# Performance work log

Hardware: AMD Instinct MI355X
Metric: run time of the kernel (lower is better)

## Reference

```python
import jax, jax.numpy as jnp
import numpy as np

ALPHA = 0.2  # LeakyReLU negative slope
NEG_INF = -9e15


def setup_inputs() -> dict:
    key = jax.random.key(0)
    k1, k2, k3, k4 = jax.random.split(key, 4)
    N, IN_F, OUT_F, H = 8192, 256, 128, 2
    HD = OUT_F // H
    h = jax.random.normal(k1, (N, IN_F), dtype=jnp.float32)
    adj = jax.random.randint(k2, (N, N), 0, 2, dtype=jnp.int32)
    # xavier_uniform with gain=1.414
    g = 1.414
    limW = g * np.sqrt(6.0 / (IN_F + HD))
    W = jax.random.uniform(k3, (H, IN_F, HD), jnp.float32, -limW, limW)
    lima = g * np.sqrt(6.0 / (2 * HD + 1))
    a = jax.random.uniform(k4, (H, 2 * HD, 1), jnp.float32, -lima, lima)
    return {"h": h, "adj": adj, "W": W, "a": a}


def reference(h, adj, W, a):
    # Wh: (H, N, HD)
    Wh = jnp.einsum('ni,hid->hnd', h, W)
    HD = W.shape[-1]
    a1 = a[:, :HD, 0]   # (H, HD) -> applied to Wh_i
    a2 = a[:, HD:, 0]   # (H, HD) -> applied to Wh_j
    # a . [Wh_i || Wh_j] == a1.Wh_i + a2.Wh_j ; avoids the (N,N,2HD) tensor
    f1 = jnp.einsum('hnd,hd->hn', Wh, a1)  # (H, N)
    f2 = jnp.einsum('hnd,hd->hn', Wh, a2)  # (H, N)
    e = jax.nn.leaky_relu(f1[:, :, None] + f2[:, None, :], ALPHA)  # (H, N, N)
    mask = (adj > 0)[None, :, :]
    e = jnp.where(mask, e, NEG_INF)
    attention = jax.nn.softmax(e, axis=-1)  # (H, N, N)
    # dropout is identity in eval mode
    h_prime = jnp.einsum('hnm,hmd->hnd', attention, Wh)  # (H, N, HD)
    N = h.shape[0]
    h_prime = jnp.transpose(h_prime, (1, 0, 2)).reshape(N, -1)  # concat heads
    return jax.nn.elu(h_prime)
```

## Files before the change

### kernel.cpp

```cpp
#include <hip/hip_runtime.h>
#include <stdint.h>

#define N_NODES 8192
#define IN_F    256
#define HD      64
#define NH      2
#define MS      4
#define NT      ((N_NODES / MS) / 64)
#define ALPHA   0.2f

typedef __attribute__((ext_vector_type(8))) short bf16x8s;
typedef __attribute__((ext_vector_type(4))) float f32x4;

#define OFF_U      0
#define OFF_WFRAG  4096
#define OFF_F1     69632
#define OFF_F2     135168
#define OFF_F2MAX  200704
#define OFF_G2     200960
#define OFF_WHB    332032
#define OFF_OP     2429184
#define OFF_LP     19206400

__device__ __forceinline__ unsigned short f2bf(float x) {
  union { float f; uint32_t u; } c; c.f = x;
  uint32_t r = c.u + 0x7FFFu + ((c.u >> 16) & 1u);
  return (unsigned short)(r >> 16);
}

__global__ void gat_prep_kernel(const float* __restrict__ W, const float* __restrict__ a,
                                float* __restrict__ u, unsigned short* __restrict__ wfrag)
{
  int idx = blockIdx.x * 256 + threadIdx.x;
  if (idx < 32768) {
    int j = idx & 7, lane = (idx >> 3) & 63, ks = (idx >> 9) & 7, Dt = idx >> 12;
    int k  = ks * 32 + ((lane >> 4) << 3) + j;
    int dp = Dt * 16 + (lane & 15);
    int hh = dp >> 6, d = dp & 63;
    wfrag[idx] = f2bf(W[(size_t)(hh * IN_F + k) * HD + d]);
  } else if (idx < 32768 + NH * 2 * IN_F) {
    int i2 = idx - 32768;
    int i = i2 & 255, v = (i2 >> 8) & 1, h = i2 >> 9;
    const float* Wp = W + (size_t)(h * IN_F + i) * HD;
    const float* ap = a + h * 2 * HD + v * HD;
    float s = 0.f;
    for (int d = 0; d < HD; ++d) s += Wp[d] * ap[d];
    u[(h * 2 + v) * IN_F + i] = s;
  }
}

__global__ __launch_bounds__(256) void gat_f12_kernel(const float* __restrict__ hmat,
    const float* __restrict__ u, float* __restrict__ f1, float* __restrict__ f2,
    float2* __restrict__ g2)
{
  int n = blockIdx.x * 4 + (threadIdx.x >> 6);
  int l = threadIdx.x & 63;
  float4 hv = *(const float4*)(hmat + (size_t)n * IN_F + l * 4);
  float s[4];
#pragma unroll
  for (int q = 0; q < 4; ++q) {
    float4 uv = *(const float4*)(u + q * IN_F + l * 4);
    s[q] = hv.x * uv.x + hv.y * uv.y + hv.z * uv.z + hv.w * uv.w;
  }
#pragma unroll
  for (int off = 1; off < 64; off <<= 1) {
#pragma unroll
    for (int q = 0; q < 4; ++q) s[q] += __shfl_xor(s[q], off);
  }
  if (l == 0) {
    f1[n] = s[0];           f2[n] = s[1];
    f1[N_NODES + n] = s[2]; f2[N_NODES + n] = s[3];
    g2[n]           = make_float2(__expf(s[1]), __expf(ALPHA * s[1]));
    g2[N_NODES + n] = make_float2(__expf(s[3]), __expf(ALPHA * s[3]));
  }
}

__global__ void gat_f2max_kernel(const float* __restrict__ f2, float* __restrict__ f2m)
{
  int h = blockIdx.x;
  float m = -1e30f;
  for (int i = threadIdx.x; i < N_NODES; i += 256) m = fmaxf(m, f2[h * N_NODES + i]);
#pragma unroll
  for (int off = 1; off < 64; off <<= 1) m = fmaxf(m, __shfl_xor(m, off));
  __shared__ float red[4];
  if ((threadIdx.x & 63) == 0) red[threadIdx.x >> 6] = m;
  __syncthreads();
  if (threadIdx.x == 0) f2m[h] = fmaxf(fmaxf(red[0], red[1]), fmaxf(red[2], red[3]));
}

__global__ __launch_bounds__(256) void gat_wh_kernel(const float* __restrict__ hmat,
    const unsigned short* __restrict__ wfrag, unsigned short* __restrict__ whb)
{
  int tid = threadIdx.x;
  int w = tid >> 6, l = tid & 63;
  int n0 = blockIdx.x * 64;
  int row = n0 + w * 16 + (l & 15);
  f32x4 acc[8] = {};
#pragma unroll
  for (int ks = 0; ks < 8; ++ks) {
    const float* ap = hmat + (size_t)row * IN_F + ks * 32 + ((l >> 4) << 3);
    float av[8];
    *(float4*)&av[0] = *(const float4*)ap;
    *(float4*)&av[4] = *(const float4*)(ap + 4);
    bf16x8s af;
#pragma unroll
    for (int j = 0; j < 8; ++j) af[j] = (short)f2bf(av[j]);
#pragma unroll
    for (int Dt = 0; Dt < 8; ++Dt) {
      bf16x8s bfv = *(const bf16x8s*)(wfrag + ((size_t)(Dt * 8 + ks) * 64 + l) * 8);
      acc[Dt] = __builtin_amdgcn_mfma_f32_16x16x32_bf16(af, bfv, acc[Dt], 0, 0, 0);
    }
  }
  int Tm = blockIdx.x;
  int s  = w >> 1;
  int lb = ((w & 1) * 2 + ((l >> 4) >> 1)) * 16 + (l & 15);
  int jh = (l >> 4) & 1;
#pragma unroll
  for (int Dt = 0; Dt < 8; ++Dt) {
    int hh = Dt >> 2, D = Dt & 3;
    ushort4 pk;
    pk.x = f2bf(acc[Dt][0]); pk.y = f2bf(acc[Dt][1]);
    pk.z = f2bf(acc[Dt][2]); pk.w = f2bf(acc[Dt][3]);
    size_t off = ((((size_t)(hh * 128 + Tm) * 2 + s) * 4 + D) * 64 + lb) * 8 + jh * 4;
    *(ushort4*)(whb + off) = pk;
  }
}

__global__ __launch_bounds__(256) void gat_attn_kernel(
    const int* __restrict__ adj, const unsigned short* __restrict__ whb,
    const float* __restrict__ f1, const float2* __restrict__ g2,
    const float* __restrict__ f2max, float* __restrict__ Opart, float* __restrict__ Lpart)
{
  int bx = blockIdx.x;
  int split = bx & (MS - 1);
  int T = bx >> 2;
  int tid = threadIdx.x;
  int w = tid >> 6, l = tid & 63;
  int n0 = T * 64;
  int row = n0 + w * 16 + (l & 15);
  int mbase = split * (N_NODES / MS);
  int koff = (l >> 4) << 3;

  float E1[NH], Ea[NH];
#pragma unroll
  for (int h = 0; h < NH; ++h) {
    float f1v = f1[h * N_NODES + row];
    float tm  = f1v + f2max[h];
    float mrow = fmaxf(tm, ALPHA * tm);
    E1[h] = __expf(f1v - mrow);
    Ea[h] = __expf(ALPHA * f1v - mrow);
  }

  __shared__ float4 gl[2048];
  __shared__ uint4  wbuf[1024];

  {
    const float4* s0 = (const float4*)(g2 + mbase);
    const float4* s1 = (const float4*)(g2 + N_NODES + mbase);
#pragma unroll
    for (int i = 0; i < 4; ++i) {
      gl[i * 256 + tid]        = s0[i * 256 + tid];
      gl[1024 + i * 256 + tid] = s1[i * 256 + tid];
    }
  }

  const int* adjr = adj + (size_t)row * N_NODES + mbase + koff;
  const uint4* ws0 = (const uint4*)(whb + ((size_t)(0 * 128 + (mbase >> 6))) * 4096);
  const uint4* ws1 = (const uint4*)(whb + ((size_t)(1 * 128 + (mbase >> 6))) * 4096);

  int4 raA0 = *(const int4*)(adjr);      int4 raA1 = *(const int4*)(adjr + 4);
  int4 raA2 = *(const int4*)(adjr + 32); int4 raA3 = *(const int4*)(adjr + 36);
  int4 raB0 = *(const int4*)(adjr + 64); int4 raB1 = *(const int4*)(adjr + 68);
  int4 raB2 = *(const int4*)(adjr + 96); int4 raB3 = *(const int4*)(adjr + 100);
  uint4 rw0 = ws0[tid], rw1 = ws0[tid + 256];
  uint4 rw2 = ws1[tid], rw3 = ws1[tid + 256];

  f32x4 acc[NH][4] = {};
  float lsum[NH] = {0.f, 0.f};

#pragma unroll 2
  for (int mt = 0; mt < NT; ++mt) {
    __syncthreads();
    wbuf[tid]       = rw0; wbuf[tid + 256] = rw1;
    wbuf[tid + 512] = rw2; wbuf[tid + 768] = rw3;

    int aj[16];
    *(int4*)&aj[0]  = raA0; *(int4*)&aj[4]  = raA1;
    *(int4*)&aj[8]  = raA2; *(int4*)&aj[12] = raA3;
    raA0 = raB0; raA1 = raB1; raA2 = raB2; raA3 = raB3;
    if (mt + 2 < NT) {
      const int* ap = adjr + (mt + 2) * 64;
      raB0 = *(const int4*)ap;        raB1 = *(const int4*)(ap + 4);
      raB2 = *(const int4*)(ap + 32); raB3 = *(const int4*)(ap + 36);
    }
    if (mt + 1 < NT) {
      const uint4* wp0 = ws0 + (size_t)(mt + 1) * 512;
      const uint4* wp1 = ws1 + (size_t)(mt + 1) * 512;
      rw0 = wp0[tid]; rw1 = wp0[tid + 256];
      rw2 = wp1[tid]; rw3 = wp1[tid + 256];
    }
    __syncthreads();

#pragma unroll
    for (int h = 0; h < NH; ++h) {
      float E1h = E1[h], Eah = Ea[h];
      bf16x8s af[2];
#pragma unroll
      for (int s = 0; s < 2; ++s) {
        const float4* gp = &gl[h * 1024 + ((mt * 64 + s * 32 + koff) >> 1)];
        float ps = 0.f;
#pragma unroll
        for (int k = 0; k < 4; ++k) {
          float4 gv = gp[k];
          int a0 = aj[s * 8 + 2 * k], a1 = aj[s * 8 + 2 * k + 1];
          float p0 = (a0 > 0) ? fmaxf(E1h * gv.x, Eah * gv.y) : 0.f;
          float p1 = (a1 > 0) ? fmaxf(E1h * gv.z, Eah * gv.w) : 0.f;
          ps += p0 + p1;
          af[s][2 * k]     = (short)f2bf(p0);
          af[s][2 * k + 1] = (short)f2bf(p1);
        }
        lsum[h] += ps;
      }
      const unsigned short* lb = (const unsigned short*)wbuf + h * 4096;
#pragma unroll
      for (int s = 0; s < 2; ++s)
#pragma unroll
        for (int D = 0; D < 4; ++D) {
          bf16x8s bfv = *(const bf16x8s*)&lb[(s * 4 + D) * 512 + l * 8];
          acc[h][D] = __builtin_amdgcn_mfma_f32_16x16x32_bf16(af[s], bfv, acc[h][D], 0, 0, 0);
        }
    }
  }

#pragma unroll
  for (int h = 0; h < NH; ++h) {
    float ls = lsum[h];
    ls += __shfl_xor(ls, 16);
    ls += __shfl_xor(ls, 32);
    if (l < 16) Lpart[((size_t)(split * NH + h) << 13) + n0 + w * 16 + l] = ls;
    float* op = Opart + (size_t)(split * NH + h) * N_NODES * HD;
#pragma unroll
    for (int D = 0; D < 4; ++D)
#pragma unroll
      for (int r = 0; r < 4; ++r) {
        int orow = n0 + w * 16 + ((l >> 4) << 2) + r;
        op[(size_t)orow * HD + D * 16 + (l & 15)] = acc[h][D][r];
      }
  }
}

__global__ __launch_bounds__(256) void gat_final_kernel(const float* __restrict__ Opart,
    const float* __restrict__ Lpart, float* __restrict__ out)
{
  int idx = blockIdx.x * 256 + threadIdx.x;
  int n = idx >> 7, c = idx & 127;
  int h = c >> 6, d = c & 63;
  float v = 0.f, ls = 0.f;
#pragma unroll
  for (int sp = 0; sp < MS; ++sp) {
    v  += Opart[((size_t)(sp * NH + h) * N_NODES + n) * HD + d];
    ls += Lpart[(size_t)(sp * NH + h) * N_NODES + n];
  }
  float r = v / fmaxf(ls, 1e-30f);
  out[idx] = (r > 0.f) ? r : (__expf(r) - 1.f);
}

extern "C" void kernel_launch(void* const* d_in, const int* in_sizes, int n_in,
                              void* d_out, int out_size, void* d_ws, size_t ws_size,
                              hipStream_t stream)
{
  const float* hmat = (const float*)d_in[0];
  const int*   adj  = (const int*)d_in[1];
  const float* W    = (const float*)d_in[2];
  const float* a    = (const float*)d_in[3];
  float* out = (float*)d_out;
  char* ws = (char*)d_ws;

  float* u             = (float*)(ws + OFF_U);
  unsigned short* wfrg = (unsigned short*)(ws + OFF_WFRAG);
  float* f1            = (float*)(ws + OFF_F1);
  float* f2            = (float*)(ws + OFF_F2);
  float* f2m           = (float*)(ws + OFF_F2MAX);
  float2* g2           = (float2*)(ws + OFF_G2);
  unsigned short* whb  = (unsigned short*)(ws + OFF_WHB);
  float* Opart         = (float*)(ws + OFF_OP);
  float* Lpart         = (float*)(ws + OFF_LP);

  gat_prep_kernel <<<132, 256, 0, stream>>>(W, a, u, wfrg);
  gat_f12_kernel  <<<N_NODES / 4, 256, 0, stream>>>(hmat, u, f1, f2, g2);
  gat_f2max_kernel<<<NH, 256, 0, stream>>>(f2, f2m);
  gat_wh_kernel   <<<N_NODES / 64, 256, 0, stream>>>(hmat, wfrg, whb);
  gat_attn_kernel <<<128 * MS, 256, 0, stream>>>(adj, whb, f1, g2, f2m, Opart, Lpart);
  gat_final_kernel<<<out_size / 256, 256, 0, stream>>>(Opart, Lpart, out);
}
```

Baseline: 109.8 us.

## Process two row groups per attention block to reuse Wh tiles, double split count

```diff
diff --git a/kernel.cpp b/kernel.cpp
--- a/kernel.cpp
+++ b/kernel.cpp
@@ -1,11 +1,12 @@
 #include <hip/hip_runtime.h>
+#include <hip/hip_bf16.h>
 #include <stdint.h>
 
 #define N_NODES 8192
 #define IN_F    256
 #define HD      64
 #define NH      2
-#define MS      4
+#define MS      8
 #define NT      ((N_NODES / MS) / 64)
 #define ALPHA   0.2f
 
@@ -20,12 +21,16 @@
 #define OFF_G2     200960
 #define OFF_WHB    332032
 #define OFF_OP     2429184
-#define OFF_LP     19206400
+#define OFF_LP     35983616
 
 __device__ __forceinline__ unsigned short f2bf(float x) {
   union { float f; uint32_t u; } c; c.f = x;
   uint32_t r = c.u + 0x7FFFu + ((c.u >> 16) & 1u);
   return (unsigned short)(r >> 16);
+}
+__device__ __forceinline__ short f2bfs(float x) {
+  __hip_bfloat16 b = __float2bfloat16(x);
+  return __builtin_bit_cast(short, b);
 }
 
 __global__ void gat_prep_kernel(const float* __restrict__ W, const float* __restrict__ a,
@@ -104,7 +109,7 @@
     *(float4*)&av[4] = *(const float4*)(ap + 4);
     bf16x8s af;
 #pragma unroll
-    for (int j = 0; j < 8; ++j) af[j] = (short)f2bf(av[j]);
+    for (int j = 0; j < 8; ++j) af[j] = f2bfs(av[j]);
 #pragma unroll
     for (int Dt = 0; Dt < 8; ++Dt) {
       bf16x8s bfv = *(const bf16x8s*)(wfrag + ((size_t)(Dt * 8 + ks) * 64 + l) * 8);
@@ -126,73 +131,68 @@
   }
 }
 
-__global__ __launch_bounds__(256) void gat_attn_kernel(
+#define LOADADJ(d0, d1, d2, d3, p, base) \
+  d0 = *(const int4*)((p) + (base));      d1 = *(const int4*)((p) + (base) + 4); \
+  d2 = *(const int4*)((p) + (base) + 32); d3 = *(const int4*)((p) + (base) + 36);
+
+__global__ __launch_bounds__(256, 2) void gat_attn_kernel(
     const int* __restrict__ adj, const unsigned short* __restrict__ whb,
     const float* __restrict__ f1, const float2* __restrict__ g2,
     const float* __restrict__ f2max, float* __restrict__ Opart, float* __restrict__ Lpart)
 {
   int bx = blockIdx.x;
   int split = bx & (MS - 1);
-  int T = bx >> 2;
+  int T = bx >> 3;
   int tid = threadIdx.x;
   int w = tid >> 6, l = tid & 63;
-  int n0 = T * 64;
-  int row = n0 + w * 16 + (l & 15);
+  int n0 = T * 128;
+  int rbase = n0 + w * 16 + (l & 15);
   int mbase = split * (N_NODES / MS);
   int koff = (l >> 4) << 3;
 
-  float E1[NH], Ea[NH];
-#pragma unroll
-  for (int h = 0; h < NH; ++h) {
-    float f1v = f1[h * N_NODES + row];
-    float tm  = f1v + f2max[h];
-    float mrow = fmaxf(tm, ALPHA * tm);
-    E1[h] = __expf(f1v - mrow);
-    Ea[h] = __expf(ALPHA * f1v - mrow);
-  }
-
-  __shared__ float4 gl[2048];
+  float E1[NH][2], Ea[NH][2];
+#pragma unroll
+  for (int h = 0; h < NH; ++h)
+#pragma unroll
+    for (int rg = 0; rg < 2; ++rg) {
+      float f1v = f1[h * N_NODES + rbase + rg * 64];
+      float tm  = f1v + f2max[h];
+      float mrow = fmaxf(tm, ALPHA * tm);
+      E1[h][rg] = __expf(f1v - mrow);
+      Ea[h][rg] = __expf(ALPHA * f1v - mrow);
+    }
+
+  __shared__ float4 gl[2][512];
   __shared__ uint4  wbuf[1024];
 
   {
     const float4* s0 = (const float4*)(g2 + mbase);
     const float4* s1 = (const float4*)(g2 + N_NODES + mbase);
-#pragma unroll
-    for (int i = 0; i < 4; ++i) {
-      gl[i * 256 + tid]        = s0[i * 256 + tid];
-      gl[1024 + i * 256 + tid] = s1[i * 256 + tid];
-    }
-  }
-
-  const int* adjr = adj + (size_t)row * N_NODES + mbase + koff;
-  const uint4* ws0 = (const uint4*)(whb + ((size_t)(0 * 128 + (mbase >> 6))) * 4096);
-  const uint4* ws1 = (const uint4*)(whb + ((size_t)(1 * 128 + (mbase >> 6))) * 4096);
-
-  int4 raA0 = *(const int4*)(adjr);      int4 raA1 = *(const int4*)(adjr + 4);
-  int4 raA2 = *(const int4*)(adjr + 32); int4 raA3 = *(const int4*)(adjr + 36);
-  int4 raB0 = *(const int4*)(adjr + 64); int4 raB1 = *(const int4*)(adjr + 68);
-  int4 raB2 = *(const int4*)(adjr + 96); int4 raB3 = *(const int4*)(adjr + 100);
+    gl[0][tid] = s0[tid]; gl[0][tid + 256] = s0[tid + 256];
+    gl[1][tid] = s1[tid]; gl[1][tid + 256] = s1[tid + 256];
+  }
+
+  const int* adjr0 = adj + (size_t)rbase * N_NODES + mbase + koff;
+  const int* adjr1 = adjr0 + (size_t)64 * N_NODES;
+  const uint4* ws0 = (const uint4*)(whb + ((size_t)(mbase >> 6)) * 4096);
+  const uint4* ws1 = (const uint4*)(whb + ((size_t)(128 + (mbase >> 6))) * 4096);
+
+  int4 cA0, cA1, cA2, cA3, cB0, cB1, cB2, cB3;
+  int4 nA0, nA1, nA2, nA3, nB0, nB1, nB2, nB3;
+  LOADADJ(cA0, cA1, cA2, cA3, adjr0, 0);
+  LOADADJ(cB0, cB1, cB2, cB3, adjr1, 0);
+  LOADADJ(nA0, nA1, nA2, nA3, adjr0, 64);
+  LOADADJ(nB0, nB1, nB2, nB3, adjr1, 64);
   uint4 rw0 = ws0[tid], rw1 = ws0[tid + 256];
   uint4 rw2 = ws1[tid], rw3 = ws1[tid + 256];
 
-  f32x4 acc[NH][4] = {};
-  float lsum[NH] = {0.f, 0.f};
-
-#pragma unroll 2
+  f32x4 acc[NH][2][4] = {};
+  float lsum[NH][2] = {};
+
   for (int mt = 0; mt < NT; ++mt) {
     __syncthreads();
     wbuf[tid]       = rw0; wbuf[tid + 256] = rw1;
     wbuf[tid + 512] = rw2; wbuf[tid + 768] = rw3;
-
-    int aj[16];
-    *(int4*)&aj[0]  = raA0; *(int4*)&aj[4]  = raA1;
-    *(int4*)&aj[8]  = raA2; *(int4*)&aj[12] = raA3;
-    raA0 = raB0; raA1 = raB1; raA2 = raB2; raA3 = raB3;
-    if (mt + 2 < NT) {
-      const int* ap = adjr + (mt + 2) * 64;
-      raB0 = *(const int4*)ap;        raB1 = *(const int4*)(ap + 4);
-      raB2 = *(const int4*)(ap + 32); raB3 = *(const int4*)(ap + 36);
-    }
     if (mt + 1 < NT) {
       const uint4* wp0 = ws0 + (size_t)(mt + 1) * 512;
       const uint4* wp1 = ws1 + (size_t)(mt + 1) * 512;
@@ -201,25 +201,35 @@
     }
     __syncthreads();
 
+    int ajA[16], ajB[16];
+    *(int4*)&ajA[0] = cA0; *(int4*)&ajA[4]  = cA1;
+    *(int4*)&ajA[8] = cA2; *(int4*)&ajA[12] = cA3;
+    *(int4*)&ajB[0] = cB0; *(int4*)&ajB[4]  = cB1;
+    *(int4*)&ajB[8] = cB2; *(int4*)&ajB[12] = cB3;
+
 #pragma unroll
     for (int h = 0; h < NH; ++h) {
-      float E1h = E1[h], Eah = Ea[h];
-      bf16x8s af[2];
+      bf16x8s afA[2], afB[2];
 #pragma unroll
       for (int s = 0; s < 2; ++s) {
-        const float4* gp = &gl[h * 1024 + ((mt * 64 + s * 32 + koff) >> 1)];
-        float ps = 0.f;
+        const float4* gp = &gl[h][(mt * 64 + s * 32 + koff) >> 1];
+        float psA = 0.f, psB = 0.f;
 #pragma unroll
         for (int k = 0; k < 4; ++k) {
           float4 gv = gp[k];
-          int a0 = aj[s * 8 + 2 * k], a1 = aj[s * 8 + 2 * k + 1];
-          float p0 = (a0 > 0) ? fmaxf(E1h * gv.x, Eah * gv.y) : 0.f;
-          float p1 = (a1 > 0) ? fmaxf(E1h * gv.z, Eah * gv.w) : 0.f;
-          ps += p0 + p1;
-          af[s][2 * k]     = (short)f2bf(p0);
-          af[s][2 * k + 1] = (short)f2bf(p1);
+          float m1x = E1[h][0] * gv.x, max_ = Ea[h][0] * gv.y;
+          float pA0 = (ajA[s * 8 + 2 * k]     > 0) ? fmaxf(m1x, max_) : 0.f;
+          float m1z = E1[h][0] * gv.z, maz = Ea[h][0] * gv.w;
+          float pA1 = (ajA[s * 8 + 2 * k + 1] > 0) ? fmaxf(m1z, maz) : 0.f;
+          float n1x = E1[h][1] * gv.x, nax = Ea[h][1] * gv.y;
+          float pB0 = (ajB[s * 8 + 2 * k]     > 0) ? fmaxf(n1x, nax) : 0.f;
+          float n1z = E1[h][1] * gv.z, naz = Ea[h][1] * gv.w;
+          float pB1 = (ajB[s * 8 + 2 * k + 1] > 0) ? fmaxf(n1z, naz) : 0.f;
+          psA += pA0 + pA1;  psB += pB0 + pB1;
+          afA[s][2 * k] = f2bfs(pA0); afA[s][2 * k + 1] = f2bfs(pA1);
+          afB[s][2 * k] = f2bfs(pB0); afB[s][2 * k + 1] = f2bfs(pB1);
         }
-        lsum[h] += ps;
+        lsum[h][0] += psA; lsum[h][1] += psB;
       }
       const unsigned short* lb = (const unsigned short*)wbuf + h * 4096;
 #pragma unroll
@@ -227,26 +237,36 @@
 #pragma unroll
         for (int D = 0; D < 4; ++D) {
           bf16x8s bfv = *(const bf16x8s*)&lb[(s * 4 + D) * 512 + l * 8];
-          acc[h][D] = __builtin_amdgcn_mfma_f32_16x16x32_bf16(af[s], bfv, acc[h][D], 0, 0, 0);
+          acc[h][0][D] = __builtin_amdgcn_mfma_f32_16x16x32_bf16(afA[s], bfv, acc[h][0][D], 0, 0, 0);
+          acc[h][1][D] = __builtin_amdgcn_mfma_f32_16x16x32_bf16(afB[s], bfv, acc[h][1][D], 0, 0, 0);
         }
     }
-  }
-
-#pragma unroll
-  for (int h = 0; h < NH; ++h) {
-    float ls = lsum[h];
-    ls += __shfl_xor(ls, 16);
-    ls += __shfl_xor(ls, 32);
-    if (l < 16) Lpart[((size_t)(split * NH + h) << 13) + n0 + w * 16 + l] = ls;
-    float* op = Opart + (size_t)(split * NH + h) * N_NODES * HD;
-#pragma unroll
-    for (int D = 0; D < 4; ++D)
-#pragma unroll
-      for (int r = 0; r < 4; ++r) {
-        int orow = n0 + w * 16 + ((l >> 4) << 2) + r;
-        op[(size_t)orow * HD + D * 16 + (l & 15)] = acc[h][D][r];
-      }
-  }
+
+    cA0 = nA0; cA1 = nA1; cA2 = nA2; cA3 = nA3;
+    cB0 = nB0; cB1 = nB1; cB2 = nB2; cB3 = nB3;
+    if (mt + 2 < NT) {
+      LOADADJ(nA0, nA1, nA2, nA3, adjr0, (mt + 2) * 64);
+      LOADADJ(nB0, nB1, nB2, nB3, adjr1, (mt + 2) * 64);
+    }
+  }
+
+#pragma unroll
+  for (int h = 0; h < NH; ++h)
+#pragma unroll
+    for (int rg = 0; rg < 2; ++rg) {
+      float ls = lsum[h][rg];
+      ls += __shfl_xor(ls, 16);
+      ls += __shfl_xor(ls, 32);
+      if (l < 16) Lpart[((size_t)(split * NH + h) << 13) + n0 + rg * 64 + w * 16 + l] = ls;
+      float* op = Opart + (size_t)(split * NH + h) * N_NODES * HD;
+#pragma unroll
+      for (int D = 0; D < 4; ++D)
+#pragma unroll
+        for (int r = 0; r < 4; ++r) {
+          int orow = n0 + rg * 64 + w * 16 + ((l >> 4) << 2) + r;
+          op[(size_t)orow * HD + D * 16 + (l & 15)] = acc[h][rg][D][r];
+        }
+    }
 }
 
 __global__ __launch_bounds__(256) void gat_final_kernel(const float* __restrict__ Opart,
@@ -290,6 +310,6 @@
   gat_f12_kernel  <<<N_NODES / 4, 256, 0, stream>>>(hmat, u, f1, f2, g2);
   gat_f2max_kernel<<<NH, 256, 0, stream>>>(f2, f2m);
   gat_wh_kernel   <<<N_NODES / 64, 256, 0, stream>>>(hmat, wfrg, whb);
-  gat_attn_kernel <<<128 * MS, 256, 0, stream>>>(adj, whb, f1, g2, f2m, Opart, Lpart);
+  gat_attn_kernel <<<64 * MS, 256, 0, stream>>>(adj, whb, f1, g2, f2m, Opart, Lpart);
   gat_final_kernel<<<out_size / 256, 256, 0, stream>>>(Opart, Lpart, out);
 }
```

After: 109.4 us. No clear change (-0.3%).

## Double the column splits and read Wh fragments straight from global memory

Applied to the files above, without the earlier changes.

```diff
diff --git a/kernel.cpp b/kernel.cpp
--- a/kernel.cpp
+++ b/kernel.cpp
@@ -1,12 +1,14 @@
 #include <hip/hip_runtime.h>
+#include <hip/hip_bf16.h>
 #include <stdint.h>
 
 #define N_NODES 8192
 #define IN_F    256
 #define HD      64
 #define NH      2
-#define MS      4
-#define NT      ((N_NODES / MS) / 64)
+#define MS      8
+#define SLICE   1024
+#define NT      16
 #define ALPHA   0.2f
 
 typedef __attribute__((ext_vector_type(8))) short bf16x8s;
@@ -20,12 +22,16 @@
 #define OFF_G2     200960
 #define OFF_WHB    332032
 #define OFF_OP     2429184
-#define OFF_LP     19206400
+#define OFF_LP     35983616
 
 __device__ __forceinline__ unsigned short f2bf(float x) {
   union { float f; uint32_t u; } c; c.f = x;
   uint32_t r = c.u + 0x7FFFu + ((c.u >> 16) & 1u);
   return (unsigned short)(r >> 16);
+}
+__device__ __forceinline__ short f2bfs(float x) {
+  __hip_bfloat16 b = __float2bfloat16(x);
+  return __builtin_bit_cast(short, b);
 }
 
 __global__ void gat_prep_kernel(const float* __restrict__ W, const float* __restrict__ a,
@@ -104,7 +110,7 @@
     *(float4*)&av[4] = *(const float4*)(ap + 4);
     bf16x8s af;
 #pragma unroll
-    for (int j = 0; j < 8; ++j) af[j] = (short)f2bf(av[j]);
+    for (int j = 0; j < 8; ++j) af[j] = f2bfs(av[j]);
 #pragma unroll
     for (int Dt = 0; Dt < 8; ++Dt) {
       bf16x8s bfv = *(const bf16x8s*)(wfrag + ((size_t)(Dt * 8 + ks) * 64 + l) * 8);
@@ -126,20 +132,30 @@
   }
 }
 
-__global__ __launch_bounds__(256) void gat_attn_kernel(
+__global__ __launch_bounds__(256, 3) void gat_attn_kernel(
     const int* __restrict__ adj, const unsigned short* __restrict__ whb,
     const float* __restrict__ f1, const float2* __restrict__ g2,
     const float* __restrict__ f2max, float* __restrict__ Opart, float* __restrict__ Lpart)
 {
   int bx = blockIdx.x;
   int split = bx & (MS - 1);
-  int T = bx >> 2;
+  int T = bx >> 3;
   int tid = threadIdx.x;
   int w = tid >> 6, l = tid & 63;
   int n0 = T * 64;
   int row = n0 + w * 16 + (l & 15);
-  int mbase = split * (N_NODES / MS);
+  int mbase = split * SLICE;
   int koff = (l >> 4) << 3;
+  int cb = mbase >> 6;
+
+  __shared__ float4 gl[2][512];
+
+  {
+    const float4* s0 = (const float4*)(g2 + mbase);
+    const float4* s1 = (const float4*)(g2 + N_NODES + mbase);
+    gl[0][tid] = s0[tid]; gl[0][tid + 256] = s0[tid + 256];
+    gl[1][tid] = s1[tid]; gl[1][tid + 256] = s1[tid + 256];
+  }
 
   float E1[NH], Ea[NH];
 #pragma unroll
@@ -151,82 +167,64 @@
     Ea[h] = __expf(ALPHA * f1v - mrow);
   }
 
-  __shared__ float4 gl[2048];
-  __shared__ uint4  wbuf[1024];
-
-  {
-    const float4* s0 = (const float4*)(g2 + mbase);
-    const float4* s1 = (const float4*)(g2 + N_NODES + mbase);
-#pragma unroll
-    for (int i = 0; i < 4; ++i) {
-      gl[i * 256 + tid]        = s0[i * 256 + tid];
-      gl[1024 + i * 256 + tid] = s1[i * 256 + tid];
-    }
-  }
+  __syncthreads();
 
   const int* adjr = adj + (size_t)row * N_NODES + mbase + koff;
-  const uint4* ws0 = (const uint4*)(whb + ((size_t)(0 * 128 + (mbase >> 6))) * 4096);
-  const uint4* ws1 = (const uint4*)(whb + ((size_t)(1 * 128 + (mbase >> 6))) * 4096);
-
-  int4 raA0 = *(const int4*)(adjr);      int4 raA1 = *(const int4*)(adjr + 4);
-  int4 raA2 = *(const int4*)(adjr + 32); int4 raA3 = *(const int4*)(adjr + 36);
-  int4 raB0 = *(const int4*)(adjr + 64); int4 raB1 = *(const int4*)(adjr + 68);
-  int4 raB2 = *(const int4*)(adjr + 96); int4 raB3 = *(const int4*)(adjr + 100);
-  uint4 rw0 = ws0[tid], rw1 = ws0[tid + 256];
-  uint4 rw2 = ws1[tid], rw3 = ws1[tid + 256];
+  const uint4* whb4 = (const uint4*)whb;
+
+  int4 c0 = *(const int4*)(adjr);      int4 c1 = *(const int4*)(adjr + 4);
+  int4 c2 = *(const int4*)(adjr + 32); int4 c3 = *(const int4*)(adjr + 36);
+  int4 x0 = *(const int4*)(adjr + 64); int4 x1 = *(const int4*)(adjr + 68);
+  int4 x2 = *(const int4*)(adjr + 96); int4 x3 = *(const int4*)(adjr + 100);
 
   f32x4 acc[NH][4] = {};
   float lsum[NH] = {0.f, 0.f};
 
 #pragma unroll 2
   for (int mt = 0; mt < NT; ++mt) {
-    __syncthreads();
-    wbuf[tid]       = rw0; wbuf[tid + 256] = rw1;
-    wbuf[tid + 512] = rw2; wbuf[tid + 768] = rw3;
+    uint4 wfr[NH][2][4];
+#pragma unroll
+    for (int h = 0; h < NH; ++h)
+#pragma unroll
+      for (int s = 0; s < 2; ++s)
+#pragma unroll
+        for (int D = 0; D < 4; ++D)
+          wfr[h][s][D] = whb4[(size_t)((((h * 128 + cb + mt) * 2 + s) * 4 + D) * 64 + l)];
 
     int aj[16];
-    *(int4*)&aj[0]  = raA0; *(int4*)&aj[4]  = raA1;
-    *(int4*)&aj[8]  = raA2; *(int4*)&aj[12] = raA3;
-    raA0 = raB0; raA1 = raB1; raA2 = raB2; raA3 = raB3;
+    *(int4*)&aj[0]  = c0; *(int4*)&aj[4]  = c1;
+    *(int4*)&aj[8]  = c2; *(int4*)&aj[12] = c3;
+    c0 = x0; c1 = x1; c2 = x2; c3 = x3;
     if (mt + 2 < NT) {
       const int* ap = adjr + (mt + 2) * 64;
-      raB0 = *(const int4*)ap;        raB1 = *(const int4*)(ap + 4);
-      raB2 = *(const int4*)(ap + 32); raB3 = *(const int4*)(ap + 36);
+      x0 = *(const int4*)ap;        x1 = *(const int4*)(ap + 4);
+      x2 = *(const int4*)(ap + 32); x3 = *(const int4*)(ap + 36);
     }
-    if (mt + 1 < NT) {
-      const uint4* wp0 = ws0 + (size_t)(mt + 1) * 512;
-      const uint4* wp1 = ws1 + (size_t)(mt + 1) * 512;
-      rw0 = wp0[tid]; rw1 = wp0[tid + 256];
-      rw2 = wp1[tid]; rw3 = wp1[tid + 256];
-    }
-    __syncthreads();
 
 #pragma unroll
     for (int h = 0; h < NH; ++h) {
-      float E1h = E1[h], Eah = Ea[h];
       bf16x8s af[2];
 #pragma unroll
       for (int s = 0; s < 2; ++s) {
-        const float4* gp = &gl[h * 1024 + ((mt * 64 + s * 32 + koff) >> 1)];
+        const float4* gp = &gl[h][(mt * 64 + s * 32 + koff) >> 1];
         float ps = 0.f;
 #pragma unroll
         for (int k = 0; k < 4; ++k) {
           float4 gv = gp[k];
-          int a0 = aj[s * 8 + 2 * k], a1 = aj[s * 8 + 2 * k + 1];
-          float p0 = (a0 > 0) ? fmaxf(E1h * gv.x, Eah * gv.y) : 0.f;
-          float p1 = (a1 > 0) ? fmaxf(E1h * gv.z, Eah * gv.w) : 0.f;
+          float v0 = fmaxf(E1[h] * gv.x, Ea[h] * gv.y);
+          float v1 = fmaxf(E1[h] * gv.z, Ea[h] * gv.w);
+          float p0 = (aj[s * 8 + 2 * k]     > 0) ? v0 : 0.f;
+          float p1 = (aj[s * 8 + 2 * k + 1] > 0) ? v1 : 0.f;
           ps += p0 + p1;
-          af[s][2 * k]     = (short)f2bf(p0);
-          af[s][2 * k + 1] = (short)f2bf(p1);
+          af[s][2 * k] = f2bfs(p0); af[s][2 * k + 1] = f2bfs(p1);
         }
         lsum[h] += ps;
       }
-      const unsigned short* lb = (const unsigned short*)wbuf + h * 4096;
 #pragma unroll
       for (int s = 0; s < 2; ++s)
 #pragma unroll
         for (int D = 0; D < 4; ++D) {
-          bf16x8s bfv = *(const bf16x8s*)&lb[(s * 4 + D) * 512 + l * 8];
+          bf16x8s bfv = __builtin_bit_cast(bf16x8s, wfr[h][s][D]);
           acc[h][D] = __builtin_amdgcn_mfma_f32_16x16x32_bf16(af[s], bfv, acc[h][D], 0, 0, 0);
         }
     }
```

Result: slower. 302.5 us (+175.5%).
